# Performance work log

Hardware: AMD Instinct MI355X
Metric: run time of the kernel (lower is better)

Reference implementation:

```python
import jax, jax.numpy as jnp
import numpy as np

NUM_HEADS = 8

def _ln(x, w, b, eps=1e-5):
    m = x.mean(-1, keepdims=True)
    v = ((x - m) ** 2).mean(-1, keepdims=True)
    return (x - m) / jnp.sqrt(v + eps) * w + b

def _l2n(x, axis=-1, eps=1e-12):
    n = jnp.linalg.norm(x, axis=axis, keepdims=True)
    return x / jnp.maximum(n, eps)

def setup_inputs() -> dict:
    key = jax.random.key(0)
    ks = jax.random.split(key, 30)
    B, N, C, nc, t = 2, 4096, 256, 150, 3
    Hh = Ww = 64
    hid = 4 * C
    s = 0.02
    inp = {}
    inp['x'] = jax.random.normal(ks[0], (B, N, C), jnp.float32)
    inp['z'] = jax.random.normal(ks[1], (B, nc, (t + 1) * N), jnp.float32)
    inp['mem'] = jax.random.normal(ks[2], (B * t, N, C), jnp.float32)
    inp['clustering_w'] = s * jax.random.normal(ks[3], (nc, C), jnp.float32)
    inp['prompt1'] = jax.random.normal(ks[4], (nc,), jnp.float32)
    inp['tdt1'] = jnp.eye(nc, dtype=jnp.float32) + s * jax.random.normal(ks[5], (nc, nc), jnp.float32)
    inp['prompt2'] = jax.random.normal(ks[6], (nc,), jnp.float32)
    inp['tdt2'] = jnp.eye(nc, dtype=jnp.float32) + s * jax.random.normal(ks[7], (nc, nc), jnp.float32)
    inp['sim_alpha'] = jnp.ones((1,), jnp.float32)
    inp['sim_beta'] = jnp.zeros((1,), jnp.float32)
    inp['q_w'] = s * jax.random.normal(ks[8], (C, C), jnp.float32)
    inp['q_b'] = s * jax.random.normal(ks[9], (C,), jnp.float32)
    inp['k_w'] = s * jax.random.normal(ks[10], (C, C), jnp.float32)
    inp['k_b'] = s * jax.random.normal(ks[11], (C,), jnp.float32)
    inp['v_w'] = s * jax.random.normal(ks[12], (C, C), jnp.float32)
    inp['v_b'] = s * jax.random.normal(ks[13], (C,), jnp.float32)
    inp['proj_w'] = s * jax.random.normal(ks[14], (C, C), jnp.float32)
    inp['proj_b'] = s * jax.random.normal(ks[15], (C,), jnp.float32)
    inp['norm_w'] = jnp.ones((C,), jnp.float32)
    inp['norm_b'] = jnp.zeros((C,), jnp.float32)
    inp['fc1_w'] = s * jax.random.normal(ks[16], (hid, C), jnp.float32)
    inp['fc1_b'] = s * jax.random.normal(ks[17], (hid,), jnp.float32)
    inp['dw_w'] = s * jax.random.normal(ks[18], (hid, 1, 3, 3), jnp.float32)
    inp['dw_b'] = s * jax.random.normal(ks[19], (hid,), jnp.float32)
    inp['fc2_w'] = s * jax.random.normal(ks[20], (C, hid), jnp.float32)
    inp['fc2_b'] = s * jax.random.normal(ks[21], (C,), jnp.float32)
    inp['H'] = Hh
    inp['W'] = Ww
    inp['t'] = t
    return inp

def _forward(x, z, mem, clustering_w, prompt1, tdt1, prompt2, tdt2, sim_alpha, sim_beta,
             q_w, q_b, k_w, k_b, v_w, v_b, proj_w, proj_b, norm_w, norm_b,
             fc1_w, fc1_b, dw_w, dw_b, fc2_w, fc2_b, H, W, t):
    B, N, C = x.shape
    nc = clustering_w.shape[0]
    res = x
    T = t + 1
    # cat memory frames with current frame: [(B*T), N, C]
    xf = jnp.concatenate([mem.reshape(B, t, N, C), x[:, None]], axis=1).reshape(B * T, N, C)
    # clustering head: (SRPS approximated as identity) 1x1 conv dim->num_clusters
    cl = jnp.einsum('bnc,kc->bkn', xf, clustering_w)            # [(B*T), nc, N]
    cl = cl.reshape(B, T, nc, N).transpose(0, 2, 1, 3).reshape(B, nc, T * N)
    # top-down prompt modulation of z and cluster logits
    zc = z.transpose(0, 2, 1)                                   # [B, T*N, nc]
    cos = _l2n(zc, -1) @ _l2n(prompt1[None, :, None], axis=1)   # [B, T*N, 1]
    zc = (zc * jnp.clip(cos, 0.0, 1.0)) @ tdt1
    clc = cl.transpose(0, 2, 1)
    cos = _l2n(clc, -1) @ _l2n(prompt2[None, :, None], axis=1)
    clc = (clc * jnp.clip(cos, 0.0, 1.0)) @ tdt2
    cluster_x_z = ((clc + zc) * 0.5).transpose(0, 2, 1)          # [B, nc, T*N]
    # inner_center: per-frame soft assignment -> cluster centers
    center = cluster_x_z.reshape(B, nc, T, N).transpose(0, 2, 1, 3)  # [B, T, nc, N]
    assigned_results = center
    soft = jax.nn.softmax(center, axis=-1)
    cx = xf.reshape(B, T, N, C)
    cen = jnp.einsum('btkn,btnc->btkc', soft, cx)               # [B, T, nc, C]
    last, prev = cen[:, -1], cen[:, :-1]                        # [B,nc,C], [B,t,nc,C]
    dot = jnp.einsum('bkc,btkc->btk', last, prev)
    denom = jnp.maximum(jnp.linalg.norm(last, axis=-1)[:, None] * jnp.linalg.norm(prev, axis=-1), 1e-8)
    gate = jax.nn.sigmoid(sim_beta + sim_alpha * (dot / denom))  # [B, t, nc]
    C_in = last + (gate[..., None] * prev).sum(axis=1)          # [B, nc, C]
    C_in = _ln(C_in, norm_w, norm_b)
    # cross attention: tokens query cluster centers
    hd = C // NUM_HEADS
    q = (res @ q_w.T + q_b) * (1.0 / np.sqrt(hd))
    k = C_in @ k_w.T + k_b
    v = C_in @ v_w.T + v_b
    q = q.reshape(B, N, NUM_HEADS, hd).transpose(0, 2, 1, 3)
    k = k.reshape(B, nc, NUM_HEADS, hd).transpose(0, 2, 1, 3)
    v = v.reshape(B, nc, NUM_HEADS, hd).transpose(0, 2, 1, 3)
    attn = jax.nn.softmax(jnp.einsum('bhnd,bhkd->bhnk', q, k), axis=-1)
    o = jnp.einsum('bhnk,bhkd->bhnd', attn, v).transpose(0, 2, 1, 3).reshape(B, N, C)
    o = o @ proj_w.T + proj_b
    out = res + _ln(o, norm_w, norm_b)
    # MLP with depthwise conv
    h = out @ fc1_w.T + fc1_b                                   # [B, N, 4C]
    hid = h.shape[-1]
    h_img = h.transpose(0, 2, 1).reshape(B, hid, H, W)
    h_img = jax.lax.conv_general_dilated(h_img, dw_w, (1, 1), 'SAME',
                                         feature_group_count=hid,
                                         dimension_numbers=('NCHW', 'OIHW', 'NCHW'))
    h_img = h_img + dw_b[None, :, None, None]
    h = h_img.reshape(B, hid, N).transpose(0, 2, 1)
    h = jax.nn.gelu(h, approximate=False) @ fc2_w.T + fc2_b
    out = out + _ln(h, norm_w, norm_b)
    return out, cluster_x_z, assigned_results

def reference(x, z, mem, clustering_w, prompt1, tdt1, prompt2, tdt2, sim_alpha, sim_beta,
              q_w, q_b, k_w, k_b, v_w, v_b, proj_w, proj_b, norm_w, norm_b,
              fc1_w, fc1_b, dw_w, dw_b, fc2_w, fc2_b, H, W, t):
    return _forward(x, z, mem, clustering_w, prompt1, tdt1, prompt2, tdt2, sim_alpha, sim_beta,
                    q_w, q_b, k_w, k_b, v_w, v_b, proj_w, proj_b, norm_w, norm_b,
                    fc1_w, fc1_b, dw_w, dw_b, fc2_w, fc2_b, H, W, t)
```

## Files before the change

### kernel.cpp

```cpp
#include <hip/hip_runtime.h>
#include <math.h>


typedef __attribute__((ext_vector_type(8))) short bf16x8;
typedef __attribute__((ext_vector_type(4))) float f32x4;

__device__ __forceinline__ short f2b(float f) {
  union { float f; unsigned int u; } c; c.f = f;
  unsigned int r = (c.u + 0x7fffu + ((c.u >> 16) & 1u)) >> 16;
  return (short)r;
}

__device__ __forceinline__ float bred_sum(float v, float* red) {
  int tid = threadIdx.x;
  red[tid] = v; __syncthreads();
  #pragma unroll
  for (int s = 128; s > 0; s >>= 1) {
    if (tid < s) red[tid] += red[tid + s];
    __syncthreads();
  }
  float r = red[0]; __syncthreads();
  return r;
}

// ... 32 lines not shown
      float4 v1 = *(const float4*)&ap[4];
      float4 v2 = *(const float4*)&ap[8];
      float4 v3 = *(const float4*)&ap[12];
      bf16x8 w0, w1;
      w0[0] = f2b(v0.x); w0[1] = f2b(v0.y); w0[2] = f2b(v0.z); w0[3] = f2b(v0.w);
      w0[4] = f2b(v1.x); w0[5] = f2b(v1.y); w0[6] = f2b(v1.z); w0[7] = f2b(v1.w);
      w1[0] = f2b(v2.x); w1[1] = f2b(v2.y); w1[2] = f2b(v2.z); w1[3] = f2b(v2.w);
      w1[4] = f2b(v3.x); w1[5] = f2b(v3.y); w1[6] = f2b(v3.z); w1[7] = f2b(v3.w);
      *(bf16x8*)&As[row * 72 + sk] = w0;
      *(bf16x8*)&As[row * 72 + sk + 8] = w1;
    }
    {
      const float* wp = &W[(size_t)(n0 + sr) * K + k0 + sk];
      float4 v0 = *(const float4*)&wp[0];
      float4 v1 = *(const float4*)&wp[4];
      float4 v2 = *(const float4*)&wp[8];
      float4 v3 = *(const float4*)&wp[12];
      bf16x8 w0, w1;
      w0[0] = f2b(v0.x); w0[1] = f2b(v0.y); w0[2] = f2b(v0.z); w0[3] = f2b(v0.w);
      w0[4] = f2b(v1.x); w0[5] = f2b(v1.y); w0[6] = f2b(v1.z); w0[7] = f2b(v1.w);
      w1[0] = f2b(v2.x); w1[1] = f2b(v2.y); w1[2] = f2b(v2.z); w1[3] = f2b(v2.w);
      w1[4] = f2b(v3.x); w1[5] = f2b(v3.y); w1[6] = f2b(v3.z); w1[7] = f2b(v3.w);
      *(bf16x8*)&Bs[sr * 72 + sk] = w0;
      *(bf16x8*)&Bs[sr * 72 + sk + 8] = w1;
    }
    __syncthreads();
    #pragma unroll
    for (int ks = 0; ks < 2; ++ks) {
      const int kofs = ks * 32 + k8;
      bf16x8 af0 = *(const bf16x8*)&As[(wm * 64 +  0 + t16) * 72 + kofs];
      bf16x8 af1 = *(const bf16x8*)&As[(wm * 64 + 16 + t16) * 72 + kofs];
      bf16x8 af2 = *(const bf16x8*)&As[(wm * 64 + 32 + t16) * 72 + kofs];
      bf16x8 af3 = *(const bf16x8*)&As[(wm * 64 + 48 + t16) * 72 + kofs];
      bf16x8 bf0 = *(const bf16x8*)&Bs[(wn * 32 +  0 + t16) * 72 + kofs];
      bf16x8 bf1 = *(const bf16x8*)&Bs[(wn * 32 + 16 + t16) * 72 + kofs];
      acc[0][0] = __builtin_amdgcn_mfma_f32_16x16x32_bf16(af0, bf0, acc[0][0], 0, 0, 0);
      acc[1][0] = __builtin_amdgcn_mfma_f32_16x16x32_bf16(af1, bf0, acc[1][0], 0, 0, 0);
      acc[2][0] = __builtin_amdgcn_mfma_f32_16x16x32_bf16(af2, bf0, acc[2][0], 0, 0, 0);
      acc[3][0] = __builtin_amdgcn_mfma_f32_16x16x32_bf16(af3, bf0, acc[3][0], 0, 0, 0);
      acc[0][1] = __builtin_amdgcn_mfma_f32_16x16x32_bf16(af0, bf1, acc[0][1], 0, 0, 0);
      acc[1][1] = __builtin_amdgcn_mfma_f32_16x16x32_bf16(af1, bf1, acc[1][1], 0, 0, 0);
      acc[2][1] = __builtin_amdgcn_mfma_f32_16x16x32_bf16(af2, bf1, acc[2][1], 0, 0, 0);
      acc[3][1] = __builtin_amdgcn_mfma_f32_16x16x32_bf16(af3, bf1, acc[3][1], 0, 0, 0);
    }
    __syncthreads();
  }
  const int r4 = (lane >> 4) * 4;
  #pragma unroll
  for (int ni = 0; ni < 2; ++ni) {
    const int gcol = n0 + wn * 32 + ni * 16 + t16;
    const float bb = bias[gcol];
    #pragma unroll
    for (int mi = 0; mi < 4; ++mi) {
      #pragma unroll
      for (int r = 0; r < 4; ++r) {
        const int gm = m0 + wm * 64 + mi * 16 + r4 + r;
        out[(size_t)gm * N + gcol] = alpha * (acc[mi][ni][r] + bb);
      }
    }
  }
}

__global__ __launch_bounds__(256) void prep_bt(
    const float* __restrict__ cw, const float* __restrict__ tdt2, const float* __restrict__ tdt1,
    short* __restrict__ cwb, short* __restrict__ TT)
{
  int idx = blockIdx.x * 256 + threadIdx.x;
  if (idx < 160 * 256) {
    int kc = idx >> 8, k = idx & 255;
    float v = (kc < 150) ? cw[kc * 256 + k] : 0.f;
    cwb[idx] = f2b(v);
  }
  if (idx < 160 * 320) {
    int kc = idx / 320, kk = idx - kc * 320;
    float t = 0.f;
    if (kc < 150) {
      if (kk < 150) t = tdt2[kk * 150 + kc];
      else if (kk >= 160 && kk < 310) t = tdt1[(kk - 160) * 150 + kc];
    }
    TT[idx] = f2b(t);
  }
}

__global__ __launch_bounds__(256) void cl_cos_prep(
    const float* __restrict__ x, const float* __restrict__ mem,
    const short* __restrict__ cwb, const float* __restrict__ p2,
    short* __restrict__ Acat)
{
  __shared__ __align__(16) short ls[64][168];
  __shared__ float p2s[160];
  const int tid = threadIdx.x;
  const int r0 = blockIdx.x * 64;
  const int b = r0 >> 14, ti = (r0 >> 12) & 3;
  const int nn0 = r0 & 4095;
  const float* Ab = ((ti < 3) ? (mem + (size_t)(b * 3 + ti) * 4096 * 256)
                              : (x + (size_t)b * 4096 * 256)) + (size_t)nn0 * 256;
  const int wave = tid >> 6, lane = tid & 63;
  const int t16 = lane & 15, quad = lane >> 4, k8 = quad * 8;
  if (tid < 160) p2s[tid] = (tid < 150) ? p2[tid] : 0.f;
  __syncthreads();

  f32x4 acc[10];
  #pragma unroll
  for (int i = 0; i < 10; ++i) acc[i] = (f32x4){0.f, 0.f, 0.f, 0.f};
  const float* ap = Ab + (size_t)(wave * 16 + t16) * 256 + k8;
  const short* bp = cwb + t16 * 256 + k8;
  #pragma unroll 2
  for (int ks = 0; ks < 8; ++ks) {
    float4 v0 = *(const float4*)&ap[ks * 32];
    float4 v1 = *(const float4*)&ap[ks * 32 + 4];
    bf16x8 a;
    a[0] = f2b(v0.x); a[1] = f2b(v0.y); a[2] = f2b(v0.z); a[3] = f2b(v0.w);
    a[4] = f2b(v1.x); a[5] = f2b(v1.y); a[6] = f2b(v1.z); a[7] = f2b(v1.w);
    #pragma unroll
    for (int nf = 0; nf < 10; ++nf) {
      bf16x8 bv = *(const bf16x8*)&bp[nf * 4096 + ks * 32];
      acc[nf] = __builtin_amdgcn_mfma_f32_16x16x32_bf16(a, bv, acc[nf], 0, 0, 0);
    }
  }
  float d[4] = {0.f, 0.f, 0.f, 0.f}, s[4] = {0.f, 0.f, 0.f, 0.f};
  float pn = 0.f;
  #pragma unroll
  for (int nf = 0; nf < 10; ++nf) {
    float a2 = p2s[nf * 16 + t16];
    pn += a2 * a2;
    #pragma unroll
    for (int r = 0; r < 4; ++r) {
      float v = acc[nf][r];
      d[r] = fmaf(v, a2, d[r]);
      s[r] = fmaf(v, v, s[r]);
    }
  }
  #pragma unroll
  for (int off = 1; off < 16; off <<= 1) {
    pn += __shfl_xor(pn, off);
    #pragma unroll
    for (int r = 0; r < 4; ++r) {
      d[r] += __shfl_xor(d[r], off);
      s[r] += __shfl_xor(s[r], off);
    }
  }
  const float spn = fmaxf(sqrtf(pn), 1e-12f);
  float cs[4];
  #pragma unroll
  for (int r = 0; r < 4; ++r) {
    float c = d[r] / (fmaxf(sqrtf(s[r]), 1e-12f) * spn);
    cs[r] = fminf(fmaxf(c, 0.f), 1.f);
  }
  #pragma unroll
  for (int nf = 0; nf < 10; ++nf)
    #pragma unroll
    for (int r = 0; r < 4; ++r)
      ls[wave * 16 + quad * 4 + r][nf * 16 + t16] = f2b(acc[nf][r] * cs[r]);
  __syncthreads();
  #pragma unroll
  for (int i = 0; i < 5; ++i) {
    const int idx = tid + i * 256;
    const int m = idx / 20, seg = idx - m * 20;
    *(bf16x8*)&Acat[(size_t)(r0 + m) * 320 + seg * 8] = *(const bf16x8*)&ls[m][seg * 8];
  }
}

__global__ __launch_bounds__(256) void z_prep(
    const float* __restrict__ z, const float* __restrict__ p1, short* __restrict__ Acat)
{
  __shared__ __align__(16) float zs[160][68];
  __shared__ float sred[4][16][9];
  __shared__ float czs[64];
  const int tid = threadIdx.x;
  const int C0 = blockIdx.x * 64;
  const int b = C0 >> 14;
  const int mmb = C0 & 16383;
  const int kr = tid >> 4, c4 = (tid & 15) * 4;
  float d[4] = {0.f, 0.f, 0.f, 0.f}, sv[4] = {0.f, 0.f, 0.f, 0.f};
  float pn = 0.f;
  #pragma unroll
  for (int it = 0; it < 10; ++it) {
    const int k = it * 16 + kr;
    float4 v = make_float4(0.f, 0.f, 0.f, 0.f);
    float a = 0.f;
    if (k < 150) {
      v = *(const float4*)&z[((size_t)b * 150 + k) * 16384 + mmb + c4];
      a = p1[k];
    }
    *(float4*)&zs[k][c4] = v;
    d[0] = fmaf(v.x, a, d[0]); d[1] = fmaf(v.y, a, d[1]);
    d[2] = fmaf(v.z, a, d[2]); d[3] = fmaf(v.w, a, d[3]);
    sv[0] = fmaf(v.x, v.x, sv[0]); sv[1] = fmaf(v.y, v.y, sv[1]);
    sv[2] = fmaf(v.z, v.z, sv[2]); sv[3] = fmaf(v.w, v.w, sv[3]);
    pn = fmaf(a, a, pn);
  }
  const int lane = tid & 63, wave = tid >> 6;
  #pragma unroll
  for (int off = 16; off < 64; off <<= 1) {
    pn += __shfl_xor(pn, off);
    #pragma unroll
    for (int r = 0; r < 4; ++r) {
      d[r] += __shfl_xor(d[r], off);
      sv[r] += __shfl_xor(sv[r], off);
    }
  }
  if ((lane >> 4) == 0) {
    #pragma unroll
    for (int r = 0; r < 4; ++r) {
      sred[wave][lane][r] = d[r];
      sred[wave][lane][4 + r] = sv[r];
    }
    sred[wave][lane][8] = pn;
  }
  __syncthreads();
  if (tid < 64) {
    const int cg = tid >> 2, r = tid & 3;
    float dd = 0.f, ss = 0.f, pp = 0.f;
    #pragma unroll
    for (int w = 0; w < 4; ++w) {
      dd += sred[w][cg][r];
      ss += sred[w][cg][4 + r];
      pp += sred[w][cg][8];
    }
    float c = dd / (fmaxf(sqrtf(ss), 1e-12f) * fmaxf(sqrtf(pp), 1e-12f));
    czs[tid] = fminf(fmaxf(c, 0.f), 1.f);
  }
  __syncthreads();
  #pragma unroll
  for (int i = 0; i < 5; ++i) {
    const int idx = tid + i * 256;
    const int m = idx / 20, seg = idx - m * 20;
    const float cz = czs[m];
    bf16x8 w;
    #pragma unroll
    for (int j = 0; j < 8; ++j) w[j] = f2b(zs[seg * 8 + j][m] * cz);
    *(bf16x8*)&Acat[(size_t)(C0 + m) * 320 + 160 + seg * 8] = w;
  }
}

__global__ __launch_bounds__(256) void gemm_csz2(
    const short* __restrict__ Acat, const short* __restrict__ TT,
    float* __restrict__ csz, float* __restrict__ asg)
{
  const int tid = threadIdx.x;
  const int r0 = blockIdx.x * 64;
  const int b = r0 >> 14;
  const int mmg = r0 & 16383;
  const int ti = mmg >> 12, nn = mmg & 4095;
  const int wave = tid >> 6, lane = tid & 63;
  const int wm = wave & 1, wn = wave >> 1;
  const int t16 = lane & 15, quad = lane >> 4, k8 = quad * 8;
  f32x4 acc[2][5];
  #pragma unroll
  for (int i = 0; i < 2; ++i)
    #pragma unroll
    for (int j = 0; j < 5; ++j)
      acc[i][j] = (f32x4){0.f, 0.f, 0.f, 0.f};

  const short* a0p = Acat + (size_t)(r0 + wm * 32 + t16) * 320 + k8;
  const short* a1p = a0p + 16 * 320;
  const short* bp  = TT + (size_t)(wn * 80 + t16) * 320 + k8;
  #pragma unroll 2
  for (int ks = 0; ks < 10; ++ks) {
    bf16x8 a0 = *(const bf16x8*)&a0p[ks * 32];
    bf16x8 a1 = *(const bf16x8*)&a1p[ks * 32];
    #pragma unroll
    for (int nf = 0; nf < 5; ++nf) {
      bf16x8 bv = *(const bf16x8*)&bp[nf * 5120 + ks * 32];
      acc[0][nf] = __builtin_amdgcn_mfma_f32_16x16x32_bf16(a0, bv, acc[0][nf], 0, 0, 0);
      acc[1][nf] = __builtin_amdgcn_mfma_f32_16x16x32_bf16(a1, bv, acc[1][nf], 0, 0, 0);
    }
  }
  #pragma unroll
  for (int nf = 0; nf < 5; ++nf) {
    const int kc = wn * 80 + nf * 16 + t16;
    if (kc < 150) {
      #pragma unroll
      for (int mf = 0; mf < 2; ++mf) {
        const int moff = wm * 32 + mf * 16 + quad * 4;
        float4 r4;
        r4.x = 0.5f * acc[mf][nf][0];
        r4.y = 0.5f * acc[mf][nf][1];
        r4.z = 0.5f * acc[mf][nf][2];
        r4.w = 0.5f * acc[mf][nf][3];
        *(float4*)&csz[((size_t)b * 150 + kc) * 16384 + mmg + moff] = r4;
        *(float4*)&asg[(((size_t)b * 4 + ti) * 150 + kc) * 4096 + nn + moff] = r4;
      }
    }
  }
}

__global__ __launch_bounds__(256) void softmax_stats_e(
    const float* __restrict__ csz, float* __restrict__ lr_, short* __restrict__ ecsz)
{
  __shared__ float wred[8];
  const int row = blockIdx.x;
  const int bt = row / 150, k = row - bt * 150;
  const int b = bt >> 2, ti = bt & 3;
  const float* p = csz + ((size_t)b * 150 + k) * 16384 + ti * 4096;
  const int base = threadIdx.x * 16;
  float4 v[4];
  #pragma unroll
  for (int i = 0; i < 4; ++i) v[i] = *(const float4*)&p[base + i * 4];
  float mx = -1e30f;
  #pragma unroll
  for (int i = 0; i < 4; ++i)
    mx = fmaxf(mx, fmaxf(fmaxf(v[i].x, v[i].y), fmaxf(v[i].z, v[i].w)));
  #pragma unroll
  for (int off = 1; off < 64; off <<= 1) mx = fmaxf(mx, __shfl_xor(mx, off));
  const int wave = threadIdx.x >> 6, lane = threadIdx.x & 63;
  if (lane == 0) wred[wave] = mx;
  __syncthreads();
  mx = fmaxf(fmaxf(wred[0], wred[1]), fmaxf(wred[2], wred[3]));
  const float L = 1.4426950408889634f;
  float s = 0.f;
  bf16x8 e0, e1;
  #pragma unroll
  for (int i = 0; i < 2; ++i) {
    float a = exp2f((v[i].x - mx) * L);
    float bq = exp2f((v[i].y - mx) * L);
    float cq = exp2f((v[i].z - mx) * L);
    float dq = exp2f((v[i].w - mx) * L);
    s += a + bq + cq + dq;
    e0[i * 4 + 0] = f2b(a); e0[i * 4 + 1] = f2b(bq); e0[i * 4 + 2] = f2b(cq); e0[i * 4 + 3] = f2b(dq);
  }
  #pragma unroll
  for (int i = 2; i < 4; ++i) {
    float a = exp2f((v[i].x - mx) * L);
    float bq = exp2f((v[i].y - mx) * L);
    float cq = exp2f((v[i].z - mx) * L);
    float dq = exp2f((v[i].w - mx) * L);
    s += a + bq + cq + dq;
    e1[(i - 2) * 4 + 0] = f2b(a); e1[(i - 2) * 4 + 1] = f2b(bq);
    e1[(i - 2) * 4 + 2] = f2b(cq); e1[(i - 2) * 4 + 3] = f2b(dq);
  }
  #pragma unroll
  for (int off = 1; off < 64; off <<= 1) s += __shfl_xor(s, off);
  if (lane == 0) wred[4 + wave] = s;
  __syncthreads();
  short* er = ecsz + ((size_t)bt * 160 + k) * 4096 + base;
  *(bf16x8*)&er[0] = e0;
  *(bf16x8*)&er[8] = e1;
  if (threadIdx.x == 0) lr_[row] = wred[4] + wred[5] + wred[6] + wred[7];
}

__global__ __launch_bounds__(256) void gemm_cen_at(
    const short* __restrict__ ecsz, const float* __restrict__ x, const float* __restrict__ mem,
    float* __restrict__ cen)
{
  __shared__ __align__(16) short As[160 * 136];
  const int tid = threadIdx.x;
  const int chalf = blockIdx.x;
  const int bt = blockIdx.y;
  const int sp = blockIdx.z;
  const int b = bt >> 2, ti = bt & 3;
  const float* xf = (ti < 3) ? (mem + (size_t)(b * 3 + ti) * 4096 * 256)
                             : (x + (size_t)b * 4096 * 256);
  const int n0 = sp * 256;
  const int wave = tid >> 6, lane = tid & 63;
  const int t16 = lane & 15, quad = lane >> 4, k8 = quad * 8;
  const int cbase = chalf * 128 + wave * 32;

  f32x4 acc[10][2];
  #pragma unroll
  for (int i = 0; i < 10; ++i) {
    acc[i][0] = (f32x4){0.f, 0.f, 0.f, 0.f};
    acc[i][1] = (f32x4){0.f, 0.f, 0.f, 0.f};
  }

  const short* erow = ecsz + (size_t)bt * 160 * 4096 + n0;
  #pragma unroll
  for (int half = 0; half < 2; ++half) {
    #pragma unroll
    for (int p = 0; p < 10; ++p) {
      const int g = p * 256 + tid;
      const int row = g >> 4;
      const int col8 = (g & 15) * 8;
      *(bf16x8*)&As[row * 136 + col8] =
          *(const bf16x8*)&erow[(size_t)row * 4096 + half * 128 + col8];
    }
    __syncthreads();
    #pragma unroll
    for (int kc = 0; kc < 4; ++kc) {
      bf16x8 bB[2];
      #pragma unroll
      for (int nt = 0; nt < 2; ++nt) {
        bf16x8 w;
        #pragma unroll
        for (int j = 0; j < 8; ++j)
          w[j] = f2b(xf[(size_t)(n0 + half * 128 + kc * 32 + k8 + j) * 256 + cbase + nt * 16 + t16]);
        bB[nt] = w;
      }
      #pragma unroll
      for (int mt = 0; mt < 10; ++mt) {
        bf16x8 aA = *(const bf16x8*)&As[(mt * 16 + t16) * 136 + kc * 32 + k8];
        acc[mt][0] = __builtin_amdgcn_mfma_f32_16x16x32_bf16(aA, bB[0], acc[mt][0], 0, 0, 0);
        acc[mt][1] = __builtin_amdgcn_mfma_f32_16x16x32_bf16(aA, bB[1], acc[mt][1], 0, 0, 0);
      }
    }
    __syncthreads();
  }
  #pragma unroll
  for (int mt = 0; mt < 10; ++mt) {
    #pragma unroll
    for (int r = 0; r < 4; ++r) {
      const int grow = mt * 16 + quad * 4 + r;
      if (grow < 150) {
        atomicAdd(&cen[((size_t)bt * 150 + grow) * 256 + cbase + t16], acc[mt][0][r]);
        atomicAdd(&cen[((size_t)bt * 150 + grow) * 256 + cbase + 16 + t16], acc[mt][1][r]);
      }
    }
  }
}

__global__ __launch_bounds__(256) void gate_ln(
    const float* __restrict__ cen, const float* __restrict__ lr_,
    const float* __restrict__ alpha_, const float* __restrict__ beta_,
    const float* __restrict__ nw, const float* __restrict__ nb, float* __restrict__ cin)
{
  __shared__ float red[256];
  int bk = blockIdx.x;
  int b = bk / 150, k = bk % 150;
  int c = threadIdx.x;
  const float* base = cen + ((size_t)b * 4 * 150) * 256;
  const float* lrb = lr_ + (size_t)b * 4 * 150;
  float lc  = base[((size_t)3 * 150 + k) * 256 + c] / lrb[3 * 150 + k];
  float p0  = base[((size_t)0 * 150 + k) * 256 + c] / lrb[0 * 150 + k];
  float p1v = base[((size_t)1 * 150 + k) * 256 + c] / lrb[1 * 150 + k];
  float p2v = base[((size_t)2 * 150 + k) * 256 + c] / lrb[2 * 150 + k];
  float nl = bred_sum(lc * lc, red);
  float q0 = bred_sum(p0 * p0, red);
  float q1 = bred_sum(p1v * p1v, red);
  float q2 = bred_sum(p2v * p2v, red);
  float d0 = bred_sum(lc * p0, red);
  float d1 = bred_sum(lc * p1v, red);
  float d2 = bred_sum(lc * p2v, red);
  float al = alpha_[0], be = beta_[0];
  float snl = sqrtf(nl);
  float g0 = 1.f / (1.f + expf(-(be + al * (d0 / fmaxf(snl * sqrtf(q0), 1e-8f)))));
  float g1 = 1.f / (1.f + expf(-(be + al * (d1 / fmaxf(snl * sqrtf(q1), 1e-8f)))));
  float g2 = 1.f / (1.f + expf(-(be + al * (d2 / fmaxf(snl * sqrtf(q2), 1e-8f)))));
  float ci = lc + g0 * p0 + g1 * p1v + g2 * p2v;
  float mu = bred_sum(ci, red) * (1.f / 256.f);
  float df = ci - mu;
  float var = bred_sum(df * df, red) * (1.f / 256.f);
  cin[(size_t)bk * 256 + c] = df * rsqrtf(var + 1e-5f) * nw[c] + nb[c];
}

__global__ __launch_bounds__(256) void gemm_nt(
    const float* __restrict__ A, const float* __restrict__ W,
    const float* __restrict__ bias, float* __restrict__ out,
    int M, int N, int K, float alpha)
{
  __shared__ __align__(16) float As[16][132];
  __shared__ __align__(16) float Ws[16][68];
  const int tid = threadIdx.x;
  const int m0 = blockIdx.x * 128;
  const int n0 = blockIdx.y * 64;
  const int tm = tid & 15;
  const int tn = tid >> 4;
  float acc[8][4];
  #pragma unroll
  for (int i = 0; i < 8; ++i)
    #pragma unroll
    for (int j = 0; j < 4; ++j) acc[i][j] = 0.f;

  const int lr = tid >> 2;
  const int lk = (tid & 3) * 4;

  for (int k0 = 0; k0 < K; k0 += 16) {
    #pragma unroll
    for (int p = 0; p < 2; ++p) {
      int r = lr + p * 64;
      int gm = m0 + r;
      float4 v = make_float4(0.f, 0.f, 0.f, 0.f);
      if (gm < M) v = *(const float4*)&A[(size_t)gm * K + k0 + lk];
      As[lk + 0][r] = v.x; As[lk + 1][r] = v.y; As[lk + 2][r] = v.z; As[lk + 3][r] = v.w;
    }
    {
      float4 v = *(const float4*)&W[(size_t)(n0 + lr) * K + k0 + lk];
      Ws[lk + 0][lr] = v.x; Ws[lk + 1][lr] = v.y; Ws[lk + 2][lr] = v.z; Ws[lk + 3][lr] = v.w;
    }
    __syncthreads();
// ... 176 lines not shown

__global__ __launch_bounds__(256) void conv_wt(
    const float* __restrict__ w, float* __restrict__ wt)
{
  int i = blockIdx.x * 256 + threadIdx.x;
  if (i < 9216) {
    int ch = i / 9, tap = i - ch * 9;
    wt[tap * 1024 + ch] = w[i];
  }
}

__global__ __launch_bounds__(256) void conv_gelu(
    const float* __restrict__ h, const float* __restrict__ wt, const float* __restrict__ bias,
    float* __restrict__ hc)
{
  const int pix = blockIdx.x;
  const int b = pix >> 12;
  const int n = pix & 4095;
  const int y = n >> 6, xx = n & 63;
  const int c4 = threadIdx.x * 4;
  float4 acc = *(const float4*)&bias[c4];
  const float* hb = h + ((size_t)b * 4096) * 1024 + c4;
  #pragma unroll
  for (int dy = 0; dy < 3; ++dy) {
    const int yy = y + dy - 1;
    if (yy < 0 || yy > 63) continue;
    #pragma unroll
    for (int dx = 0; dx < 3; ++dx) {
      const int xv = xx + dx - 1;
      if (xv < 0 || xv > 63) continue;
      float4 hv = *(const float4*)&hb[(size_t)(yy * 64 + xv) * 1024];
      float4 wv = *(const float4*)&wt[(dy * 3 + dx) * 1024 + c4];
      acc.x = fmaf(hv.x, wv.x, acc.x);
      acc.y = fmaf(hv.y, wv.y, acc.y);
      acc.z = fmaf(hv.z, wv.z, acc.z);
      acc.w = fmaf(hv.w, wv.w, acc.w);
    }
  }
  float4 g;
  g.x = 0.5f * acc.x * (1.f + erff(acc.x * 0.70710678118654752f));
  g.y = 0.5f * acc.y * (1.f + erff(acc.y * 0.70710678118654752f));
  g.z = 0.5f * acc.z * (1.f + erff(acc.z * 0.70710678118654752f));
  g.w = 0.5f * acc.w * (1.f + erff(acc.w * 0.70710678118654752f));
  *(float4*)&hc[((size_t)b * 4096 + n) * 1024 + c4] = g;
}

extern "C" void kernel_launch(void* const* d_in, const int* in_sizes, int n_in,
                              void* d_out, int out_size, void* d_ws, size_t ws_size,
                              hipStream_t stream)
{
  (void)in_sizes; (void)n_in; (void)out_size; (void)ws_size;
  const float* x    = (const float*)d_in[0];
  const float* z    = (const float*)d_in[1];
  const float* mem  = (const float*)d_in[2];
  const float* cw   = (const float*)d_in[3];
  const float* p1   = (const float*)d_in[4];
  const float* tdt1 = (const float*)d_in[5];
  const float* p2   = (const float*)d_in[6];
  const float* tdt2 = (const float*)d_in[7];
  const float* sal  = (const float*)d_in[8];
  const float* sbe  = (const float*)d_in[9];
  const float* q_w  = (const float*)d_in[10];
  const float* q_b  = (const float*)d_in[11];
  const float* k_w  = (const float*)d_in[12];
  const float* k_b  = (const float*)d_in[13];
  const float* v_w  = (const float*)d_in[14];
  const float* v_b  = (const float*)d_in[15];
  const float* pj_w = (const float*)d_in[16];
  const float* pj_b = (const float*)d_in[17];
  const float* nw   = (const float*)d_in[18];
  const float* nb   = (const float*)d_in[19];
  const float* f1w  = (const float*)d_in[20];
  const float* f1b  = (const float*)d_in[21];
  const float* dww  = (const float*)d_in[22];
  const float* dwb  = (const float*)d_in[23];
  const float* f2w  = (const float*)d_in[24];
  const float* f2b_ = (const float*)d_in[25];

  float* out = (float*)d_out;
  float* csz = out + 2097152;
  float* asg = csz + 4915200;

  float* ws    = (float*)d_ws;
  short* Acat  = (short*)ws;
  short* ecsz  = (short*)ws;
  short* TT    = (short*)(ws + 5242880);
  short* cwb   = (short*)(ws + 5275648);
  float* lr_   = ws + 5308416;
  float* cen   = ws + 5310816;
  float* cin   = ws + 5618016;
  float* q     = ws + 5694816;
  float* ksb   = ws + 7791968;
  float* vsb   = ws + 7868768;
  float* o     = ws + 7945568;
  float* h     = ws;
  float* hc    = ws + 8388608;
  float* tmp   = ws + 16777216;
  float* out1  = ws + 18874368;
  float* wt    = ws + 20971520;

  dim3 blk(256);
  prep_bt<<<dim3(200), blk, 0, stream>>>(cw, tdt2, tdt1, cwb, TT);
  z_prep<<<dim3(512), blk, 0, stream>>>(z, p1, Acat);
  cl_cos_prep<<<dim3(512), blk, 0, stream>>>(x, mem, cwb, p2, Acat);
  gemm_csz2<<<dim3(512), blk, 0, stream>>>(Acat, TT, csz, asg);
  softmax_stats_e<<<dim3(1200), blk, 0, stream>>>(csz, lr_, ecsz);
  hipMemsetAsync(cen, 0, (size_t)1200 * 256 * sizeof(float), stream);
  gemm_cen_at<<<dim3(2, 8, 16), blk, 0, stream>>>(ecsz, x, mem, cen);
  gate_ln<<<dim3(300), blk, 0, stream>>>(cen, lr_, sal, sbe, nw, nb, cin);
  gemm_mfma<<<dim3(64, 4), blk, 0, stream>>>(x, q_w, q_b, q, 8192, 256, 256, 0.17677669529663687f);
  gemm_nt<<<dim3(3, 4), blk, 0, stream>>>(cin, k_w, k_b, ksb, 300, 256, 256, 1.f);
  gemm_nt<<<dim3(3, 4), blk, 0, stream>>>(cin, v_w, v_b, vsb, 300, 256, 256, 1.f);
  attn_mfma<<<dim3(512), blk, 0, stream>>>(q, ksb, vsb, o);
  gemm_mfma<<<dim3(64, 4), blk, 0, stream>>>(o, pj_w, pj_b, tmp, 8192, 256, 256, 1.f);
  ln_res<<<dim3(2048), blk, 0, stream>>>(tmp, x, nw, nb, out1);
  gemm_mfma<<<dim3(64, 16), blk, 0, stream>>>(out1, f1w, f1b, h, 8192, 1024, 256, 1.f);
  conv_wt<<<dim3(36), blk, 0, stream>>>(dww, wt);
  conv_gelu<<<dim3(8192), blk, 0, stream>>>(h, wt, dwb, hc);
  gemm_mfma<<<dim3(64, 4), blk, 0, stream>>>(hc, f2w, f2b_, tmp, 8192, 256, 1024, 1.f);
  ln_res<<<dim3(2048), blk, 0, stream>>>(tmp, out1, nw, nb, out);
}
```

Measured before the change: 445.5 us.

## Fuse clustering prep kernels and pre-transpose features to bf16 for centroid GEMM

Merges z_prep, cl_cos_prep and gemm_csz2 into one kernel that builds the concatenated A tile in shared memory, so the Acat intermediate never round-trips through global memory. Adds an xf_t kernel that transposes x/mem into a bf16 [C,N] layout, letting gemm_cen_at issue vector loads of B fragments instead of strided scalar fp32 gathers with per-element conversion. gemm_cen_at now covers 128 tokens per block and launches twice as many blocks. The cost is an extra transpose pass and a new workspace buffer, plus higher register and shared-memory pressure in the fused kernel.

```diff
diff --git a/kernel.cpp b/kernel.cpp
--- a/kernel.cpp
+++ b/kernel.cpp
@@ -138,205 +138,222 @@
   }
 }
 
-__global__ __launch_bounds__(256) void cl_cos_prep(
-    const float* __restrict__ x, const float* __restrict__ mem,
-    const short* __restrict__ cwb, const float* __restrict__ p2,
-    short* __restrict__ Acat)
-{
-  __shared__ __align__(16) short ls[64][168];
-  __shared__ float p2s[160];
+__global__ __launch_bounds__(256) void xf_t(
+    const float* __restrict__ x, const float* __restrict__ mem, short* __restrict__ xfT)
+{
+  __shared__ float tile[64][257];
+  const int bt = blockIdx.y;
+  const int n0 = blockIdx.x * 64;
+  const int b = bt >> 2, ti = bt & 3;
+  const float* xf = (ti < 3) ? (mem + (size_t)(b * 3 + ti) * 4096 * 256)
+                             : (x + (size_t)b * 4096 * 256);
   const int tid = threadIdx.x;
-  const int r0 = blockIdx.x * 64;
-  const int b = r0 >> 14, ti = (r0 >> 12) & 3;
-  const int nn0 = r0 & 4095;
-  const float* Ab = ((ti < 3) ? (mem + (size_t)(b * 3 + ti) * 4096 * 256)
-                              : (x + (size_t)b * 4096 * 256)) + (size_t)nn0 * 256;
-  const int wave = tid >> 6, lane = tid & 63;
-  const int t16 = lane & 15, quad = lane >> 4, k8 = quad * 8;
-  if (tid < 160) p2s[tid] = (tid < 150) ? p2[tid] : 0.f;
+  const int r = tid >> 2, cofs = (tid & 3) * 64;
+  const float* src = xf + (size_t)(n0 + r) * 256 + cofs;
+  #pragma unroll
+  for (int i = 0; i < 16; ++i) {
+    float4 v = *(const float4*)&src[i * 4];
+    tile[r][cofs + i * 4 + 0] = v.x;
+    tile[r][cofs + i * 4 + 1] = v.y;
+    tile[r][cofs + i * 4 + 2] = v.z;
+    tile[r][cofs + i * 4 + 3] = v.w;
+  }
   __syncthreads();
-
-  f32x4 acc[10];
-  #pragma unroll
-  for (int i = 0; i < 10; ++i) acc[i] = (f32x4){0.f, 0.f, 0.f, 0.f};
-  const float* ap = Ab + (size_t)(wave * 16 + t16) * 256 + k8;
-  const short* bp = cwb + t16 * 256 + k8;
-  #pragma unroll 2
-  for (int ks = 0; ks < 8; ++ks) {
-    float4 v0 = *(const float4*)&ap[ks * 32];
-    float4 v1 = *(const float4*)&ap[ks * 32 + 4];
-    bf16x8 a;
-    a[0] = f2b(v0.x); a[1] = f2b(v0.y); a[2] = f2b(v0.z); a[3] = f2b(v0.w);
-    a[4] = f2b(v1.x); a[5] = f2b(v1.y); a[6] = f2b(v1.z); a[7] = f2b(v1.w);
-    #pragma unroll
-    for (int nf = 0; nf < 10; ++nf) {
-      bf16x8 bv = *(const bf16x8*)&bp[nf * 4096 + ks * 32];
-      acc[nf] = __builtin_amdgcn_mfma_f32_16x16x32_bf16(a, bv, acc[nf], 0, 0, 0);
-    }
-  }
-  float d[4] = {0.f, 0.f, 0.f, 0.f}, s[4] = {0.f, 0.f, 0.f, 0.f};
-  float pn = 0.f;
-  #pragma unroll
-  for (int nf = 0; nf < 10; ++nf) {
-    float a2 = p2s[nf * 16 + t16];
-    pn += a2 * a2;
-    #pragma unroll
-    for (int r = 0; r < 4; ++r) {
-      float v = acc[nf][r];
-      d[r] = fmaf(v, a2, d[r]);
-      s[r] = fmaf(v, v, s[r]);
-    }
-  }
-  #pragma unroll
-  for (int off = 1; off < 16; off <<= 1) {
-    pn += __shfl_xor(pn, off);
-    #pragma unroll
-    for (int r = 0; r < 4; ++r) {
-      d[r] += __shfl_xor(d[r], off);
-      s[r] += __shfl_xor(s[r], off);
-    }
-  }
-  const float spn = fmaxf(sqrtf(pn), 1e-12f);
-  float cs[4];
-  #pragma unroll
-  for (int r = 0; r < 4; ++r) {
-    float c = d[r] / (fmaxf(sqrtf(s[r]), 1e-12f) * spn);
-    cs[r] = fminf(fmaxf(c, 0.f), 1.f);
-  }
-  #pragma unroll
-  for (int nf = 0; nf < 10; ++nf)
-    #pragma unroll
-    for (int r = 0; r < 4; ++r)
-      ls[wave * 16 + quad * 4 + r][nf * 16 + t16] = f2b(acc[nf][r] * cs[r]);
-  __syncthreads();
-  #pragma unroll
-  for (int i = 0; i < 5; ++i) {
-    const int idx = tid + i * 256;
-    const int m = idx / 20, seg = idx - m * 20;
-    *(bf16x8*)&Acat[(size_t)(r0 + m) * 320 + seg * 8] = *(const bf16x8*)&ls[m][seg * 8];
-  }
-}
-
-__global__ __launch_bounds__(256) void z_prep(
-    const float* __restrict__ z, const float* __restrict__ p1, short* __restrict__ Acat)
-{
-  __shared__ __align__(16) float zs[160][68];
+  short* dst = xfT + ((size_t)bt * 256 + tid) * 4096 + n0;
+  #pragma unroll
+  for (int seg = 0; seg < 8; ++seg) {
+    bf16x8 w;
+    #pragma unroll
+    for (int j = 0; j < 8; ++j) w[j] = f2b(tile[seg * 8 + j][tid]);
+    *(bf16x8*)&dst[seg * 8] = w;
+  }
+}
+
+__global__ __launch_bounds__(256) void fused_csz(
+    const float* __restrict__ x, const float* __restrict__ mem, const float* __restrict__ z,
+    const short* __restrict__ cwb, const short* __restrict__ TT,
+    const float* __restrict__ p1, const float* __restrict__ p2,
+    float* __restrict__ csz, float* __restrict__ asg)
+{
+  __shared__ __align__(16) short Acatile[64 * 328];
+  __shared__ float p1s[160], p2s[160];
   __shared__ float sred[4][16][9];
   __shared__ float czs[64];
-  const int tid = threadIdx.x;
-  const int C0 = blockIdx.x * 64;
-  const int b = C0 >> 14;
-  const int mmb = C0 & 16383;
-  const int kr = tid >> 4, c4 = (tid & 15) * 4;
-  float d[4] = {0.f, 0.f, 0.f, 0.f}, sv[4] = {0.f, 0.f, 0.f, 0.f};
-  float pn = 0.f;
-  #pragma unroll
-  for (int it = 0; it < 10; ++it) {
-    const int k = it * 16 + kr;
-    float4 v = make_float4(0.f, 0.f, 0.f, 0.f);
-    float a = 0.f;
-    if (k < 150) {
-      v = *(const float4*)&z[((size_t)b * 150 + k) * 16384 + mmb + c4];
-      a = p1[k];
-    }
-    *(float4*)&zs[k][c4] = v;
-    d[0] = fmaf(v.x, a, d[0]); d[1] = fmaf(v.y, a, d[1]);
-    d[2] = fmaf(v.z, a, d[2]); d[3] = fmaf(v.w, a, d[3]);
-    sv[0] = fmaf(v.x, v.x, sv[0]); sv[1] = fmaf(v.y, v.y, sv[1]);
-    sv[2] = fmaf(v.z, v.z, sv[2]); sv[3] = fmaf(v.w, v.w, sv[3]);
-    pn = fmaf(a, a, pn);
-  }
-  const int lane = tid & 63, wave = tid >> 6;
-  #pragma unroll
-  for (int off = 16; off < 64; off <<= 1) {
-    pn += __shfl_xor(pn, off);
-    #pragma unroll
-    for (int r = 0; r < 4; ++r) {
-      d[r] += __shfl_xor(d[r], off);
-      sv[r] += __shfl_xor(sv[r], off);
-    }
-  }
-  if ((lane >> 4) == 0) {
-    #pragma unroll
-    for (int r = 0; r < 4; ++r) {
-      sred[wave][lane][r] = d[r];
-      sred[wave][lane][4 + r] = sv[r];
-    }
-    sred[wave][lane][8] = pn;
-  }
-  __syncthreads();
-  if (tid < 64) {
-    const int cg = tid >> 2, r = tid & 3;
-    float dd = 0.f, ss = 0.f, pp = 0.f;
-    #pragma unroll
-    for (int w = 0; w < 4; ++w) {
-      dd += sred[w][cg][r];
-      ss += sred[w][cg][4 + r];
-      pp += sred[w][cg][8];
-    }
-    float c = dd / (fmaxf(sqrtf(ss), 1e-12f) * fmaxf(sqrtf(pp), 1e-12f));
-    czs[tid] = fminf(fmaxf(c, 0.f), 1.f);
-  }
-  __syncthreads();
-  #pragma unroll
-  for (int i = 0; i < 5; ++i) {
-    const int idx = tid + i * 256;
-    const int m = idx / 20, seg = idx - m * 20;
-    const float cz = czs[m];
-    bf16x8 w;
-    #pragma unroll
-    for (int j = 0; j < 8; ++j) w[j] = f2b(zs[seg * 8 + j][m] * cz);
-    *(bf16x8*)&Acat[(size_t)(C0 + m) * 320 + 160 + seg * 8] = w;
-  }
-}
-
-__global__ __launch_bounds__(256) void gemm_csz2(
-    const short* __restrict__ Acat, const short* __restrict__ TT,
-    float* __restrict__ csz, float* __restrict__ asg)
-{
   const int tid = threadIdx.x;
   const int r0 = blockIdx.x * 64;
   const int b = r0 >> 14;
   const int mmg = r0 & 16383;
   const int ti = mmg >> 12, nn = mmg & 4095;
+  const float* Ab = ((ti < 3) ? (mem + (size_t)(b * 3 + ti) * 4096 * 256)
+                              : (x + (size_t)b * 4096 * 256)) + (size_t)nn * 256;
   const int wave = tid >> 6, lane = tid & 63;
-  const int wm = wave & 1, wn = wave >> 1;
   const int t16 = lane & 15, quad = lane >> 4, k8 = quad * 8;
-  f32x4 acc[2][5];
-  #pragma unroll
-  for (int i = 0; i < 2; ++i)
-    #pragma unroll
-    for (int j = 0; j < 5; ++j)
-      acc[i][j] = (f32x4){0.f, 0.f, 0.f, 0.f};
-
-  const short* a0p = Acat + (size_t)(r0 + wm * 32 + t16) * 320 + k8;
-  const short* a1p = a0p + 16 * 320;
-  const short* bp  = TT + (size_t)(wn * 80 + t16) * 320 + k8;
-  #pragma unroll 2
-  for (int ks = 0; ks < 10; ++ks) {
-    bf16x8 a0 = *(const bf16x8*)&a0p[ks * 32];
-    bf16x8 a1 = *(const bf16x8*)&a1p[ks * 32];
+
+  const int kr = tid >> 4, c4 = (tid & 15) * 4;
+  float4 zv[10];
+  #pragma unroll
+  for (int it = 0; it < 10; ++it) {
+    const int k = it * 16 + kr;
+    zv[it] = make_float4(0.f, 0.f, 0.f, 0.f);
+    if (k < 150) zv[it] = *(const float4*)&z[((size_t)b * 150 + k) * 16384 + mmg + c4];
+  }
+  if (tid < 160) {
+    p2s[tid] = (tid < 150) ? p2[tid] : 0.f;
+    p1s[tid] = (tid < 150) ? p1[tid] : 0.f;
+  }
+
+  f32x4 acc[10];
+  #pragma unroll
+  for (int i = 0; i < 10; ++i) acc[i] = (f32x4){0.f, 0.f, 0.f, 0.f};
+  {
+    const float* ap = Ab + (size_t)(wave * 16 + t16) * 256 + k8;
+    const short* bp = cwb + t16 * 256 + k8;
+    #pragma unroll 2
+    for (int ks = 0; ks < 8; ++ks) {
+      float4 v0 = *(const float4*)&ap[ks * 32];
+      float4 v1 = *(const float4*)&ap[ks * 32 + 4];
+      bf16x8 a;
+      a[0] = f2b(v0.x); a[1] = f2b(v0.y); a[2] = f2b(v0.z); a[3] = f2b(v0.w);
+      a[4] = f2b(v1.x); a[5] = f2b(v1.y); a[6] = f2b(v1.z); a[7] = f2b(v1.w);
+      #pragma unroll
+      for (int nf = 0; nf < 10; ++nf) {
+        bf16x8 bv = *(const bf16x8*)&bp[nf * 4096 + ks * 32];
+        acc[nf] = __builtin_amdgcn_mfma_f32_16x16x32_bf16(a, bv, acc[nf], 0, 0, 0);
+      }
+    }
+  }
+  __syncthreads();
+
+  {
+    float d[4] = {0.f, 0.f, 0.f, 0.f}, s[4] = {0.f, 0.f, 0.f, 0.f};
+    float pn = 0.f;
+    #pragma unroll
+    for (int nf = 0; nf < 10; ++nf) {
+      float a2 = p2s[nf * 16 + t16];
+      pn += a2 * a2;
+      #pragma unroll
+      for (int r = 0; r < 4; ++r) {
+        float v = acc[nf][r];
+        d[r] = fmaf(v, a2, d[r]);
+        s[r] = fmaf(v, v, s[r]);
+      }
+    }
+    #pragma unroll
+    for (int off = 1; off < 16; off <<= 1) {
+      pn += __shfl_xor(pn, off);
+      #pragma unroll
+      for (int r = 0; r < 4; ++r) {
+        d[r] += __shfl_xor(d[r], off);
+        s[r] += __shfl_xor(s[r], off);
+      }
+    }
+    const float spn = fmaxf(sqrtf(pn), 1e-12f);
+    float cs[4];
+    #pragma unroll
+    for (int r = 0; r < 4; ++r) {
+      float c = d[r] / (fmaxf(sqrtf(s[r]), 1e-12f) * spn);
+      cs[r] = fminf(fmaxf(c, 0.f), 1.f);
+    }
+    #pragma unroll
+    for (int nf = 0; nf < 10; ++nf)
+      #pragma unroll
+      for (int r = 0; r < 4; ++r)
+        Acatile[(wave * 16 + quad * 4 + r) * 328 + nf * 16 + t16] = f2b(acc[nf][r] * cs[r]);
+  }
+
+  {
+    float d[4] = {0.f, 0.f, 0.f, 0.f}, sv[4] = {0.f, 0.f, 0.f, 0.f};
+    float pn = 0.f;
+    #pragma unroll
+    for (int it = 0; it < 10; ++it) {
+      const int k = it * 16 + kr;
+      const float a = p1s[k];
+      d[0] = fmaf(zv[it].x, a, d[0]); d[1] = fmaf(zv[it].y, a, d[1]);
+      d[2] = fmaf(zv[it].z, a, d[2]); d[3] = fmaf(zv[it].w, a, d[3]);
+      sv[0] = fmaf(zv[it].x, zv[it].x, sv[0]); sv[1] = fmaf(zv[it].y, zv[it].y, sv[1]);
+      sv[2] = fmaf(zv[it].z, zv[it].z, sv[2]); sv[3] = fmaf(zv[it].w, zv[it].w, sv[3]);
+      pn = fmaf(a, a, pn);
+    }
+    #pragma unroll
+    for (int off = 16; off < 64; off <<= 1) {
+      pn += __shfl_xor(pn, off);
+      #pragma unroll
+      for (int r = 0; r < 4; ++r) {
+        d[r] += __shfl_xor(d[r], off);
+        sv[r] += __shfl_xor(sv[r], off);
+      }
+    }
+    if ((lane >> 4) == 0) {
+      #pragma unroll
+      for (int r = 0; r < 4; ++r) {
+        sred[wave][lane][r] = d[r];
+        sred[wave][lane][4 + r] = sv[r];
+      }
+      sred[wave][lane][8] = pn;
+    }
+  }
+  __syncthreads();
+  if (tid < 64) {
+    const int cg = tid >> 2, r = tid & 3;
+    float dd = 0.f, ss = 0.f, pp = 0.f;
+    #pragma unroll
+    for (int w = 0; w < 4; ++w) {
+      dd += sred[w][cg][r];
+      ss += sred[w][cg][4 + r];
+      pp += sred[w][cg][8];
+    }
+    float c = dd / (fmaxf(sqrtf(ss), 1e-12f) * fmaxf(sqrtf(pp), 1e-12f));
+    czs[tid] = fminf(fmaxf(c, 0.f), 1.f);
+  }
+  __syncthreads();
+  {
+    const float cz0 = czs[c4 + 0], cz1 = czs[c4 + 1], cz2 = czs[c4 + 2], cz3 = czs[c4 + 3];
+    #pragma unroll
+    for (int it = 0; it < 10; ++it) {
+      const int k = it * 16 + kr;
+      Acatile[(c4 + 0) * 328 + 160 + k] = f2b(zv[it].x * cz0);
+      Acatile[(c4 + 1) * 328 + 160 + k] = f2b(zv[it].y * cz1);
+      Acatile[(c4 + 2) * 328 + 160 + k] = f2b(zv[it].z * cz2);
+      Acatile[(c4 + 3) * 328 + 160 + k] = f2b(zv[it].w * cz3);
+    }
+  }
+  __syncthreads();
+
+  {
+    const int wm = wave & 1, wn = wave >> 1;
+    f32x4 c2[2][5];
+    #pragma unroll
+    for (int i = 0; i < 2; ++i)
+      #pragma unroll
+      for (int j = 0; j < 5; ++j)
+        c2[i][j] = (f32x4){0.f, 0.f, 0.f, 0.f};
+    const short* bp = TT + (size_t)(wn * 80 + t16) * 320 + k8;
+    #pragma unroll 2
+    for (int ks = 0; ks < 10; ++ks) {
+      bf16x8 a0 = *(const bf16x8*)&Acatile[(wm * 32 + t16) * 328 + ks * 32 + k8];
+      bf16x8 a1 = *(const bf16x8*)&Acatile[(wm * 32 + 16 + t16) * 328 + ks * 32 + k8];
+      #pragma unroll
+      for (int nf = 0; nf < 5; ++nf) {
+        bf16x8 bv = *(const bf16x8*)&bp[nf * 5120 + ks * 32];
+        c2[0][nf] = __builtin_amdgcn_mfma_f32_16x16x32_bf16(a0, bv, c2[0][nf], 0, 0, 0);
+        c2[1][nf] = __builtin_amdgcn_mfma_f32_16x16x32_bf16(a1, bv, c2[1][nf], 0, 0, 0);
+      }
+    }
     #pragma unroll
     for (int nf = 0; nf < 5; ++nf) {
-      bf16x8 bv = *(const bf16x8*)&bp[nf * 5120 + ks * 32];
-      acc[0][nf] = __builtin_amdgcn_mfma_f32_16x16x32_bf16(a0, bv, acc[0][nf], 0, 0, 0);
-      acc[1][nf] = __builtin_amdgcn_mfma_f32_16x16x32_bf16(a1, bv, acc[1][nf], 0, 0, 0);
-    }
-  }
-  #pragma unroll
-  for (int nf = 0; nf < 5; ++nf) {
-    const int kc = wn * 80 + nf * 16 + t16;
-    if (kc < 150) {
-      #pragma unroll
-      for (int mf = 0; mf < 2; ++mf) {
-        const int moff = wm * 32 + mf * 16 + quad * 4;
-        float4 r4;
-        r4.x = 0.5f * acc[mf][nf][0];
-        r4.y = 0.5f * acc[mf][nf][1];
-        r4.z = 0.5f * acc[mf][nf][2];
-        r4.w = 0.5f * acc[mf][nf][3];
-        *(float4*)&csz[((size_t)b * 150 + kc) * 16384 + mmg + moff] = r4;
-        *(float4*)&asg[(((size_t)b * 4 + ti) * 150 + kc) * 4096 + nn + moff] = r4;
+      const int kc = wn * 80 + nf * 16 + t16;
+      if (kc < 150) {
+        #pragma unroll
+        for (int mf = 0; mf < 2; ++mf) {
+          const int moff = wm * 32 + mf * 16 + quad * 4;
+          float4 r4;
+          r4.x = 0.5f * c2[mf][nf][0];
+          r4.y = 0.5f * c2[mf][nf][1];
+          r4.z = 0.5f * c2[mf][nf][2];
+          r4.w = 0.5f * c2[mf][nf][3];
+          *(float4*)&csz[((size_t)b * 150 + kc) * 16384 + mmg + moff] = r4;
+          *(float4*)&asg[(((size_t)b * 4 + ti) * 150 + kc) * 4096 + nn + moff] = r4;
+        }
       }
     }
   }
@@ -397,7 +414,7 @@
 }
 
 __global__ __launch_bounds__(256) void gemm_cen_at(
-    const short* __restrict__ ecsz, const float* __restrict__ x, const float* __restrict__ mem,
+    const short* __restrict__ ecsz, const short* __restrict__ xfT,
     float* __restrict__ cen)
 {
   __shared__ __align__(16) short As[160 * 136];
@@ -405,10 +422,7 @@
   const int chalf = blockIdx.x;
   const int bt = blockIdx.y;
   const int sp = blockIdx.z;
-  const int b = bt >> 2, ti = bt & 3;
-  const float* xf = (ti < 3) ? (mem + (size_t)(b * 3 + ti) * 4096 * 256)
-                             : (x + (size_t)b * 4096 * 256);
-  const int n0 = sp * 256;
+  const int n0 = sp * 128;
   const int wave = tid >> 6, lane = tid & 63;
   const int t16 = lane & 15, quad = lane >> 4, k8 = quad * 8;
   const int cbase = chalf * 128 + wave * 32;
@@ -422,35 +436,24 @@
 
   const short* erow = ecsz + (size_t)bt * 160 * 4096 + n0;
   #pragma unroll
-  for (int half = 0; half < 2; ++half) {
-    #pragma unroll
-    for (int p = 0; p < 10; ++p) {
-      const int g = p * 256 + tid;
-      const int row = g >> 4;
-      const int col8 = (g & 15) * 8;
-      *(bf16x8*)&As[row * 136 + col8] =
-          *(const bf16x8*)&erow[(size_t)row * 4096 + half * 128 + col8];
-    }
-    __syncthreads();
-    #pragma unroll
-    for (int kc = 0; kc < 4; ++kc) {
-      bf16x8 bB[2];
-      #pragma unroll
-      for (int nt = 0; nt < 2; ++nt) {
-        bf16x8 w;
-        #pragma unroll
-        for (int j = 0; j < 8; ++j)
-          w[j] = f2b(xf[(size_t)(n0 + half * 128 + kc * 32 + k8 + j) * 256 + cbase + nt * 16 + t16]);
-        bB[nt] = w;
-      }
-      #pragma unroll
-      for (int mt = 0; mt < 10; ++mt) {
-        bf16x8 aA = *(const bf16x8*)&As[(mt * 16 + t16) * 136 + kc * 32 + k8];
-        acc[mt][0] = __builtin_amdgcn_mfma_f32_16x16x32_bf16(aA, bB[0], acc[mt][0], 0, 0, 0);
-        acc[mt][1] = __builtin_amdgcn_mfma_f32_16x16x32_bf16(aA, bB[1], acc[mt][1], 0, 0, 0);
-      }
-    }
-    __syncthreads();
+  for (int p = 0; p < 10; ++p) {
+    const int g = p * 256 + tid;
+    const int row = g >> 4;
+    const int col8 = (g & 15) * 8;
+    *(bf16x8*)&As[row * 136 + col8] = *(const bf16x8*)&erow[(size_t)row * 4096 + col8];
+  }
+  __syncthreads();
+  const short* xrow = xfT + (size_t)bt * 256 * 4096 + n0;
+  #pragma unroll
+  for (int kc = 0; kc < 4; ++kc) {
+    bf16x8 b0 = *(const bf16x8*)&xrow[(size_t)(cbase + t16) * 4096 + kc * 32 + k8];
+    bf16x8 b1 = *(const bf16x8*)&xrow[(size_t)(cbase + 16 + t16) * 4096 + kc * 32 + k8];
+    #pragma unroll
+    for (int mt = 0; mt < 10; ++mt) {
+      bf16x8 aA = *(const bf16x8*)&As[(mt * 16 + t16) * 136 + kc * 32 + k8];
+      acc[mt][0] = __builtin_amdgcn_mfma_f32_16x16x32_bf16(aA, b0, acc[mt][0], 0, 0, 0);
+      acc[mt][1] = __builtin_amdgcn_mfma_f32_16x16x32_bf16(aA, b1, acc[mt][1], 0, 0, 0);
+    }
   }
   #pragma unroll
   for (int mt = 0; mt < 10; ++mt) {
@@ -793,7 +796,6 @@
   float* asg = csz + 4915200;
 
   float* ws    = (float*)d_ws;
-  short* Acat  = (short*)ws;
   short* ecsz  = (short*)ws;
   short* TT    = (short*)(ws + 5242880);
   short* cwb   = (short*)(ws + 5275648);
@@ -804,6 +806,7 @@
   float* ksb   = ws + 7791968;
   float* vsb   = ws + 7868768;
   float* o     = ws + 7945568;
+  short* xfT   = (short*)(ws + 10042720);
   float* h     = ws;
   float* hc    = ws + 8388608;
   float* tmp   = ws + 16777216;
@@ -812,12 +815,11 @@
 
   dim3 blk(256);
   prep_bt<<<dim3(200), blk, 0, stream>>>(cw, tdt2, tdt1, cwb, TT);
-  z_prep<<<dim3(512), blk, 0, stream>>>(z, p1, Acat);
-  cl_cos_prep<<<dim3(512), blk, 0, stream>>>(x, mem, cwb, p2, Acat);
-  gemm_csz2<<<dim3(512), blk, 0, stream>>>(Acat, TT, csz, asg);
+  xf_t<<<dim3(64, 8), blk, 0, stream>>>(x, mem, xfT);
+  fused_csz<<<dim3(512), blk, 0, stream>>>(x, mem, z, cwb, TT, p1, p2, csz, asg);
   softmax_stats_e<<<dim3(1200), blk, 0, stream>>>(csz, lr_, ecsz);
   hipMemsetAsync(cen, 0, (size_t)1200 * 256 * sizeof(float), stream);
-  gemm_cen_at<<<dim3(2, 8, 16), blk, 0, stream>>>(ecsz, x, mem, cen);
+  gemm_cen_at<<<dim3(2, 8, 32), blk, 0, stream>>>(ecsz, xfT, cen);
   gate_ln<<<dim3(300), blk, 0, stream>>>(cen, lr_, sal, sbe, nw, nb, cin);
   gemm_mfma<<<dim3(64, 4), blk, 0, stream>>>(x, q_w, q_b, q, 8192, 256, 256, 0.17677669529663687f);
   gemm_nt<<<dim3(3, 4), blk, 0, stream>>>(cin, k_w, k_b, ksb, 300, 256, 256, 1.f);
```

After: 441.7 us. About the same (-0.9%).
